# Kernel tuning notes

Measured on AMD Instinct MI355X. Metric: run time of the kernel, lower is better.

## Reference

```python
import jax, jax.numpy as jnp
import numpy as np

B, TQ, TK, D, F, H = 16, 256, 256, 256, 36, 8
DK = D // H          # dk = d // h
SF = int(np.sqrt(F)) # 6
MASK_VALUE = -1e30


def setup_inputs() -> dict:
    rng = jax.random.key(0)
    ks = jax.random.split(rng, 12)
    s = 0.05
    return {
        "query": jax.random.normal(ks[0], (B, TQ, D), jnp.float32),
        "key_ts": jax.random.normal(ks[1], (B, TK, D), jnp.float32),
        "value": jax.random.normal(ks[2], (B, TK, F), jnp.float32),
        "mask": (jax.random.uniform(ks[3], (B, TK, F)) < 0.5).astype(jnp.float32),
        "Wq": jax.random.normal(ks[4], (H, D, DK), jnp.float32) * s,
        "Wk": jax.random.normal(ks[5], (H, D, DK), jnp.float32) * s,
        "Wc": jax.random.normal(ks[6], (H, D), jnp.float32) * s,
        "bc": jnp.zeros((D,), jnp.float32),
        "Wo_1": jax.random.normal(ks[7], (F, SF), jnp.float32) * s,
        "bo_1": jnp.zeros((SF,), jnp.float32),
        "Wo_2": jax.random.normal(ks[8], (SF, 1), jnp.float32) * s,
        "bo_2": jnp.zeros((D,), jnp.float32),
    }


def reference(query, key_ts, value, mask, Wq, Wk, Wc, bc, Wo_1, bo_1, Wo_2, bo_2):
    # mask: [B, Tk, F] 0/1 missingness indicator -> broadcast as [B, 1, Tk, F]
    m = mask[:, None, :, :]
    heads = []
    for j in range(Wq.shape[0]):  # fixed small head loop (h=8)
        q = query @ Wq[j]                                  # [B, Tq, dk]
        k = key_ts @ Wk[j]                                 # [B, Tk, dk]
        A = jnp.einsum('bqd,bkd->bqk', q, k)[..., None]    # [B, Tq, Tk, 1] (no 1/sqrt(dk) scaling, as in original)
        A = m * A + (1.0 - m) * MASK_VALUE                 # [B, Tq, Tk, F]
        A = jax.nn.softmax(A, axis=-2)                     # softmax over Tk, per feature
        heads.append(jnp.einsum('bqkf,bkf->bqf', A, value))  # masked weighted sum
    latent = jnp.stack(heads, axis=-1)                     # [B, Tq, F, h]
    # permute (0,2,1,3) -> [B, F, Tq, h]; dot Wc[h,d] -> [B, F, Tq, d]
    latent = jnp.tanh(jnp.einsum('bqfh,hd->bfqd', latent, Wc) + bc)
    # permute (0,2,3,1) -> [B, Tq, d, F]; Wo_1: F -> sqrt(F)
    x = jnp.tanh(jnp.einsum('bfqd,fs->bqds', latent, Wo_1) + bo_1)
    # Wo_2: sqrt(F) -> 1, squeeze, add bo_2 -> [B, Tq, d]
    x = jnp.einsum('bqds,so->bqd', x, Wo_2) + bo_2
    return x
```

## Files before the change

### kernel.cpp

```cpp
#include <hip/hip_runtime.h>

#define NB 16
#define NTQ 256
#define NTK 256
#define ND 256
#define NF 36
#define NH 8
#define NDK 32
#define NSF 6

typedef __attribute__((ext_vector_type(8))) short short8;
typedef __attribute__((ext_vector_type(4))) float f32x4;
#define MFMA16(a,b,c) __builtin_amdgcn_mfma_f32_16x16x32_bf16(a,b,c,0,0,0)

#define WQTH_OFF 0u
#define WQTL_OFF (WQTH_OFF + 131072u)
#define WKTH_OFF (WQTH_OFF + 262144u)
#define WKTL_OFF (WQTH_OFF + 393216u)
#define RT_OFF   (WQTH_OFF + 524288u)
#define QPH_OFF  (2u*1024*1024)
#define QPL_OFF  (6u*1024*1024)
#define KPH_OFF  (10u*1024*1024)
#define KPL_OFF  (14u*1024*1024)
#define HD_OFF   (18u*1024*1024)

__device__ __forceinline__ short f2bf(float x){
    union { float f; unsigned u; } v; v.f = x;
    unsigned r = v.u + 0x7fffu + ((v.u >> 16) & 1u);
    return (short)(r >> 16);
}
__device__ __forceinline__ float bf2f(short s){
    union { float f; unsigned u; } v; v.u = ((unsigned)(unsigned short)s) << 16;
    return v.f;
}
__device__ __forceinline__ float fast_tanh(float x){
    float e = __expf(2.0f*x);
    return 1.0f - 2.0f/(e + 1.0f);
}
__device__ __forceinline__ short8 ld8(const short* p){ return *(const short8*)p; }

__device__ __forceinline__ void cvt8(const float* __restrict__ p, short8& h8, short8& l8){
    f32x4 a = *(const f32x4*)p;
    f32x4 c = *(const f32x4*)(p + 4);
    #pragma unroll
    for (int i = 0; i < 4; ++i){
        short h0 = f2bf(a[i]); h8[i]   = h0; l8[i]   = f2bf(a[i] - bf2f(h0));
        short h1 = f2bf(c[i]); h8[4+i] = h1; l8[4+i] = f2bf(c[i] - bf2f(h1));
    }
}

__global__ void imta_pack(const float* __restrict__ Wq, const float* __restrict__ Wk,
                          const float* __restrict__ mask, const float* __restrict__ value,
                          char* __restrict__ wsb){
    const int bid = blockIdx.x, tid = threadIdx.x;
    if (bid < 512){
        const int idx = bid*256 + tid;
        const int arr = idx >> 16, rem = idx & 65535;
        const int d = rem & 255, jdk = rem >> 8;
        const int jj = jdk >> 5, dk = jdk & 31;
        const float* __restrict__ W = arr ? Wk : Wq;
        float v = W[(jj*ND + d)*NDK + dk];
        short h = f2bf(v);
        short* oh = (short*)(wsb + (arr ? WKTH_OFF : WQTH_OFF));
        short* ol = (short*)(wsb + (arr ? WKTL_OFF : WQTL_OFF));
        oh[rem] = h; ol[rem] = f2bf(v - bf2f(h));
        return;
    }
    const int rb = bid - 512;
    const int x = rb & 15, b = rb >> 4;
    const int k = tid;
    short* rt = (short*)(wsb + RT_OFF) + b*80*256;
    #pragma unroll
    for (int r = 0; r < 5; ++r){
        const int fp = x*5 + r;
        const int f = fp >> 1;
        short o = 0;
        if (f < NF){
            float m = mask[(b*NTK + k)*NF + f];
            o = (fp & 1) ? f2bf(m) : f2bf(m * value[(b*NTK + k)*NF + f]);
        }
        rt[fp*256 + k] = o;
    }
}

__global__ __launch_bounds__(256, 8)
void imta_proj(const float* __restrict__ query, const float* __restrict__ key_ts,
               char* __restrict__ wsb){
    const int t0 = (blockIdx.x >> 2)*16, c0 = (blockIdx.x & 3)*64;
    const int side = blockIdx.y, b = blockIdx.z;
    const int tid = threadIdx.x, w = tid >> 6, lane = tid & 63;
    const int col = lane & 15, quad = lane >> 4;

    const float* __restrict__ X = side ? key_ts : query;
    const short* WH = (const short*)(wsb + (side ? WKTH_OFF : WQTH_OFF));
    const short* WL = (const short*)(wsb + (side ? WKTL_OFF : WQTL_OFF));
    short* OH = (short*)(wsb + (side ? KPH_OFF : QPH_OFF));
    short* OL = (short*)(wsb + (side ? KPL_OFF : QPL_OFF));

    const int n = c0 + w*16 + col;
    const float* xrow = X + (size_t)(b*NTQ + t0 + col)*ND;

    f32x4 acc = (f32x4)0.f;
    #pragma unroll
    for (int kb = 0; kb < 8; ++kb){
        const int dko = kb*32 + quad*8;
        short8 ah, al;
        cvt8(xrow + dko, ah, al);
        short8 bh = ld8(WH + n*ND + dko);
        short8 bl = ld8(WL + n*ND + dko);
        acc = MFMA16(al, bh, acc);
        acc = MFMA16(ah, bl, acc);
        acc = MFMA16(ah, bh, acc);
    }
    const int j = n >> 5, dk = n & 31;
    #pragma unroll
    for (int r = 0; r < 4; ++r){
        const int t = t0 + quad*4 + r;
        float v = acc[r];
        short h = f2bf(v);
        size_t o = (size_t)(((b*NH + j)*NTQ + t)*NDK + dk);
        OH[o] = h; OL[o] = f2bf(v - bf2f(h));
    }
}

__global__ __launch_bounds__(256, 8)
void imta_attn(char* __restrict__ wsb, const float* __restrict__ value){
    const int t0 = blockIdx.x*16;
    const int j = blockIdx.y, b = blockIdx.z;
    const int tid = threadIdx.x, w = tid >> 6, lane = tid & 63;
    const int col = lane & 15, quad = lane >> 4;
    __shared__ __align__(16) short sE[16*264];
    const short* QH = (const short*)(wsb + QPH_OFF) + (b*NH + j)*NTQ*NDK;
    const short* QL = (const short*)(wsb + QPL_OFF) + (b*NH + j)*NTQ*NDK;
    const short* KH = (const short*)(wsb + KPH_OFF) + (b*NH + j)*NTK*NDK;
    const short* KL = (const short*)(wsb + KPL_OFF) + (b*NH + j)*NTK*NDK;
    const short* RT = (const short*)(wsb + RT_OFF) + b*80*256;
    float* HD = (float*)(wsb + HD_OFF) + (b*NH + j)*NTQ*NF;

    short8 ah = ld8(QH + (t0 + col)*NDK + quad*8);
    short8 al = ld8(QL + (t0 + col)*NDK + quad*8);
    #pragma unroll
    for (int nt = 0; nt < 4; ++nt){
        const int key0 = w*64 + nt*16;
        short8 bh = ld8(KH + (key0 + col)*NDK + quad*8);
        short8 bl = ld8(KL + (key0 + col)*NDK + quad*8);
        f32x4 c = (f32x4)0.f;
        c = MFMA16(al, bh, c);
        c = MFMA16(ah, bl, c);
        c = MFMA16(ah, bh, c);
        const int key = key0 + col;
        #pragma unroll
        for (int r = 0; r < 4; ++r)
            sE[(quad*4 + r)*264 + key] = f2bf(__expf(c[r]));
    }
    __syncthreads();

    f32x4 accA = (f32x4)0.f, accB = (f32x4)0.f;
    #pragma unroll 2
    for (int kb = 0; kb < 8; ++kb){
        const int ko = kb*32 + quad*8;
        short8 a = *(const short8*)&sE[col*264 + ko];
        short8 bb = ld8(RT + (w*16 + col)*256 + ko);
        accA = MFMA16(a, bb, accA);
        if (w == 0){
            short8 b2 = ld8(RT + (64 + col)*256 + ko);
            accB = MFMA16(a, b2, accB);
        }
    }
    __syncthreads();
    float* sH = (float*)sE;
    #pragma unroll
    for (int r = 0; r < 4; ++r){
        float v = accA[r];
        float o = __shfl_xor(v, 1, 64);
        if (!(col & 1)){
            const int f = w*8 + (col >> 1);
            float num = v, den = o, h;
            if (den != 0.0f) h = num/den;
            else {
                float s = 0.f;
                for (int k = 0; k < NTK; ++k) s += value[(b*NTK + k)*NF + f];
                h = s * (1.0f/256.0f);
            }
            sH[(quad*4 + r)*40 + f] = h;
        }
    }
    if (w == 0){
        #pragma unroll
        for (int r = 0; r < 4; ++r){
            float v = accB[r];
            float o = __shfl_xor(v, 1, 64);
            if (!(col & 1)){
                const int f = 32 + (col >> 1);
                if (f < NF){
                    float num = v, den = o, h;
                    if (den != 0.0f) h = num/den;
                    else {
                        float s = 0.f;
                        for (int k = 0; k < NTK; ++k) s += value[(b*NTK + k)*NF + f];
                        h = s * (1.0f/256.0f);
                    }
                    sH[(quad*4 + r)*40 + f] = h;
                }
            }
        }
    }
    __syncthreads();
    for (int idx = tid; idx < 16*NF; idx += 256){
        const int q = idx/NF, f = idx - q*NF;
        HD[(t0 + q)*NF + f] = sH[q*40 + f];
    }
}

__global__ void imta_final(const float* __restrict__ Wc, const float* __restrict__ bc,
                           const float* __restrict__ Wo1, const float* __restrict__ bo1,
                           const float* __restrict__ Wo2, const float* __restrict__ bo2,
                           const float* __restrict__ hd, float* __restrict__ out){
    const int bq = blockIdx.x;
    const int b = bq >> 8, qq = bq & 255;
    const int tid = threadIdx.x;
    __shared__ float sh[NF*NH];
    __shared__ float sW1[NF*NSF];
    for (int t = tid; t < NF*NH; t += 256){
        int jj = t/NF, f = t - jj*NF;
        sh[t] = hd[((b*NH + jj)*NTQ + qq)*NF + f];
    }
    if (tid < NF*NSF) sW1[tid] = Wo1[tid];
    __syncthreads();
    const int d = tid;
    float wcr[8];
    #pragma unroll
    for (int h = 0; h < 8; ++h) wcr[h] = Wc[h*ND + d];
    const float bcd = bc[d];
    float a2[6];
    #pragma unroll
    for (int s = 0; s < 6; ++s) a2[s] = bo1[s];
    #pragma unroll
    for (int f4 = 0; f4 < NF; f4 += 4){
        float4 sv[8];
        #pragma unroll
        for (int h = 0; h < 8; ++h) sv[h] = *(const float4*)&sh[h*NF + f4];
        #pragma unroll
        for (int fi = 0; fi < 4; ++fi){
            float a = bcd;
            #pragma unroll
            for (int h = 0; h < 8; ++h)
                a = fmaf(reinterpret_cast<const float*>(&sv[h])[fi], wcr[h], a);
            float lf = fast_tanh(a);
            const int f = f4 + fi;
            #pragma unroll
            for (int s = 0; s < 6; ++s)
                a2[s] = fmaf(lf, sW1[f*NSF + s], a2[s]);
        }
    }
    float o = bo2[d];
    #pragma unroll
    for (int s = 0; s < 6; ++s)
        o = fmaf(fast_tanh(a2[s]), Wo2[s], o);
    out[(b*NTQ + qq)*ND + d] = o;
}

extern "C" void kernel_launch(void* const* d_in, const int* in_sizes, int n_in,
                              void* d_out, int out_size, void* d_ws, size_t ws_size,
                              hipStream_t stream){
    const float* query  = (const float*)d_in[0];
    const float* key_ts = (const float*)d_in[1];
    const float* value  = (const float*)d_in[2];
    const float* mask   = (const float*)d_in[3];
    const float* Wq     = (const float*)d_in[4];
    const float* Wk     = (const float*)d_in[5];
    const float* Wc     = (const float*)d_in[6];
    const float* bc     = (const float*)d_in[7];
    const float* Wo1    = (const float*)d_in[8];
    const float* bo1    = (const float*)d_in[9];
    const float* Wo2    = (const float*)d_in[10];
    const float* bo2    = (const float*)d_in[11];
    char* wsb  = (char*)d_ws;
    float* out = (float*)d_out;
    (void)in_sizes; (void)n_in; (void)out_size; (void)ws_size;

    imta_pack <<<dim3(768),      dim3(256), 0, stream>>>(Wq, Wk, mask, value, wsb);
    imta_proj <<<dim3(64, 2, 16),dim3(256), 0, stream>>>(query, key_ts, wsb);
    imta_attn <<<dim3(16, 8, 16),dim3(256), 0, stream>>>(wsb, value);
    imta_final<<<dim3(4096),     dim3(256), 0, stream>>>(Wc, bc, Wo1, bo1, Wo2, bo2,
                                                         (const float*)(wsb + HD_OFF), out);
}
```

Measured before the change: 163.5 us.

## Fuse four kernels into one persistent kernel with grid-wide barriers

Replaces the pack, projection, attention and final kernels with a single persistent kernel of 512 blocks that loops over the former work units. Phases are separated by atomic-counter grid barriers, and a memset clears the counters before each launch. This removes three kernel launch gaps and tail effects. In exchange, every phase runs on only 512 blocks, the barriers add spin-wait cost, and correctness relies on all 512 blocks being co-resident. The barrier also has a spin timeout that could let blocks proceed before the others arrive.

```diff
diff --git a/kernel.cpp b/kernel.cpp
--- a/kernel.cpp
+++ b/kernel.cpp
@@ -23,6 +23,9 @@
 #define KPH_OFF  (10u*1024*1024)
 #define KPL_OFF  (14u*1024*1024)
 #define HD_OFF   (18u*1024*1024)
+#define CNT_OFF  (24u*1024*1024)
+
+#define NBLK 512u
 
 __device__ __forceinline__ short f2bf(float x){
     union { float f; unsigned u; } v; v.f = x;
@@ -49,11 +52,35 @@
     }
 }
 
-__global__ void imta_pack(const float* __restrict__ Wq, const float* __restrict__ Wk,
-                          const float* __restrict__ mask, const float* __restrict__ value,
-                          char* __restrict__ wsb){
+__device__ __forceinline__ void gridbar(unsigned* cnt){
+    __syncthreads();
+    if (threadIdx.x == 0){
+        __threadfence();
+        __hip_atomic_fetch_add(cnt, 1u, __ATOMIC_ACQ_REL, __HIP_MEMORY_SCOPE_AGENT);
+        unsigned it = 0;
+        while (__hip_atomic_load(cnt, __ATOMIC_ACQUIRE, __HIP_MEMORY_SCOPE_AGENT) < NBLK
+               && ++it < (1u << 17))
+            __builtin_amdgcn_s_sleep(2);
+        __threadfence();
+    }
+    __syncthreads();
+}
+
+__global__ __launch_bounds__(256, 4)
+void imta_all(const float* __restrict__ query, const float* __restrict__ key_ts,
+              const float* __restrict__ value, const float* __restrict__ mask,
+              const float* __restrict__ Wq, const float* __restrict__ Wk,
+              const float* __restrict__ Wc, const float* __restrict__ bc,
+              const float* __restrict__ Wo1, const float* __restrict__ bo1,
+              const float* __restrict__ Wo2, const float* __restrict__ bo2,
+              char* __restrict__ wsb, float* __restrict__ out){
     const int bid = blockIdx.x, tid = threadIdx.x;
-    if (bid < 512){
+    const int w = tid >> 6, lane = tid & 63;
+    const int col = lane & 15, quad = lane >> 4;
+    unsigned* cnts = (unsigned*)(wsb + CNT_OFF);
+    __shared__ __align__(16) short sBuf[16*264];
+
+    {
         const int idx = bid*256 + tid;
         const int arr = idx >> 16, rem = idx & 65535;
         const int d = rem & 255, jdk = rem >> 8;
@@ -64,200 +91,203 @@
         short* oh = (short*)(wsb + (arr ? WKTH_OFF : WQTH_OFF));
         short* ol = (short*)(wsb + (arr ? WKTL_OFF : WQTL_OFF));
         oh[rem] = h; ol[rem] = f2bf(v - bf2f(h));
-        return;
-    }
-    const int rb = bid - 512;
-    const int x = rb & 15, b = rb >> 4;
-    const int k = tid;
-    short* rt = (short*)(wsb + RT_OFF) + b*80*256;
-    #pragma unroll
-    for (int r = 0; r < 5; ++r){
-        const int fp = x*5 + r;
-        const int f = fp >> 1;
-        short o = 0;
-        if (f < NF){
-            float m = mask[(b*NTK + k)*NF + f];
-            o = (fp & 1) ? f2bf(m) : f2bf(m * value[(b*NTK + k)*NF + f]);
-        }
-        rt[fp*256 + k] = o;
-    }
-}
-
-__global__ __launch_bounds__(256, 8)
-void imta_proj(const float* __restrict__ query, const float* __restrict__ key_ts,
-               char* __restrict__ wsb){
-    const int t0 = (blockIdx.x >> 2)*16, c0 = (blockIdx.x & 3)*64;
-    const int side = blockIdx.y, b = blockIdx.z;
-    const int tid = threadIdx.x, w = tid >> 6, lane = tid & 63;
-    const int col = lane & 15, quad = lane >> 4;
-
-    const float* __restrict__ X = side ? key_ts : query;
-    const short* WH = (const short*)(wsb + (side ? WKTH_OFF : WQTH_OFF));
-    const short* WL = (const short*)(wsb + (side ? WKTL_OFF : WQTL_OFF));
-    short* OH = (short*)(wsb + (side ? KPH_OFF : QPH_OFF));
-    short* OL = (short*)(wsb + (side ? KPL_OFF : QPL_OFF));
-
-    const int n = c0 + w*16 + col;
-    const float* xrow = X + (size_t)(b*NTQ + t0 + col)*ND;
-
-    f32x4 acc = (f32x4)0.f;
-    #pragma unroll
-    for (int kb = 0; kb < 8; ++kb){
-        const int dko = kb*32 + quad*8;
-        short8 ah, al;
-        cvt8(xrow + dko, ah, al);
-        short8 bh = ld8(WH + n*ND + dko);
-        short8 bl = ld8(WL + n*ND + dko);
-        acc = MFMA16(al, bh, acc);
-        acc = MFMA16(ah, bl, acc);
-        acc = MFMA16(ah, bh, acc);
-    }
-    const int j = n >> 5, dk = n & 31;
-    #pragma unroll
-    for (int r = 0; r < 4; ++r){
-        const int t = t0 + quad*4 + r;
-        float v = acc[r];
-        short h = f2bf(v);
-        size_t o = (size_t)(((b*NH + j)*NTQ + t)*NDK + dk);
-        OH[o] = h; OL[o] = f2bf(v - bf2f(h));
-    }
-}
-
-__global__ __launch_bounds__(256, 8)
-void imta_attn(char* __restrict__ wsb, const float* __restrict__ value){
-    const int t0 = blockIdx.x*16;
-    const int j = blockIdx.y, b = blockIdx.z;
-    const int tid = threadIdx.x, w = tid >> 6, lane = tid & 63;
-    const int col = lane & 15, quad = lane >> 4;
-    __shared__ __align__(16) short sE[16*264];
-    const short* QH = (const short*)(wsb + QPH_OFF) + (b*NH + j)*NTQ*NDK;
-    const short* QL = (const short*)(wsb + QPL_OFF) + (b*NH + j)*NTQ*NDK;
-    const short* KH = (const short*)(wsb + KPH_OFF) + (b*NH + j)*NTK*NDK;
-    const short* KL = (const short*)(wsb + KPL_OFF) + (b*NH + j)*NTK*NDK;
-    const short* RT = (const short*)(wsb + RT_OFF) + b*80*256;
-    float* HD = (float*)(wsb + HD_OFF) + (b*NH + j)*NTQ*NF;
-
-    short8 ah = ld8(QH + (t0 + col)*NDK + quad*8);
-    short8 al = ld8(QL + (t0 + col)*NDK + quad*8);
-    #pragma unroll
-    for (int nt = 0; nt < 4; ++nt){
-        const int key0 = w*64 + nt*16;
-        short8 bh = ld8(KH + (key0 + col)*NDK + quad*8);
-        short8 bl = ld8(KL + (key0 + col)*NDK + quad*8);
-        f32x4 c = (f32x4)0.f;
-        c = MFMA16(al, bh, c);
-        c = MFMA16(ah, bl, c);
-        c = MFMA16(ah, bh, c);
-        const int key = key0 + col;
-        #pragma unroll
-        for (int r = 0; r < 4; ++r)
-            sE[(quad*4 + r)*264 + key] = f2bf(__expf(c[r]));
-    }
-    __syncthreads();
-
-    f32x4 accA = (f32x4)0.f, accB = (f32x4)0.f;
-    #pragma unroll 2
-    for (int kb = 0; kb < 8; ++kb){
-        const int ko = kb*32 + quad*8;
-        short8 a = *(const short8*)&sE[col*264 + ko];
-        short8 bb = ld8(RT + (w*16 + col)*256 + ko);
-        accA = MFMA16(a, bb, accA);
-        if (w == 0){
-            short8 b2 = ld8(RT + (64 + col)*256 + ko);
-            accB = MFMA16(a, b2, accB);
-        }
-    }
-    __syncthreads();
-    float* sH = (float*)sE;
-    #pragma unroll
-    for (int r = 0; r < 4; ++r){
-        float v = accA[r];
-        float o = __shfl_xor(v, 1, 64);
-        if (!(col & 1)){
-            const int f = w*8 + (col >> 1);
-            float num = v, den = o, h;
-            if (den != 0.0f) h = num/den;
-            else {
-                float s = 0.f;
-                for (int k = 0; k < NTK; ++k) s += value[(b*NTK + k)*NF + f];
-                h = s * (1.0f/256.0f);
-            }
-            sH[(quad*4 + r)*40 + f] = h;
-        }
-    }
-    if (w == 0){
+    }
+    if (bid < 256){
+        const int x = bid & 15, b = bid >> 4;
+        const int k = tid;
+        short* rt = (short*)(wsb + RT_OFF) + b*80*256;
+        #pragma unroll
+        for (int r = 0; r < 5; ++r){
+            const int fp = x*5 + r;
+            const int f = fp >> 1;
+            short o = 0;
+            if (f < NF){
+                float m = mask[(b*NTK + k)*NF + f];
+                o = (fp & 1) ? f2bf(m) : f2bf(m * value[(b*NTK + k)*NF + f]);
+            }
+            rt[fp*256 + k] = o;
+        }
+    }
+    gridbar(cnts + 0);
+
+    for (int i = 0; i < 4; ++i){
+        const unsigned u = (unsigned)bid + NBLK*i;
+        const int x = u & 63, side = (u >> 6) & 1, b = u >> 7;
+        const int t0 = (x >> 2)*16, c0 = (x & 3)*64;
+        const float* __restrict__ X = side ? key_ts : query;
+        const short* WH = (const short*)(wsb + (side ? WKTH_OFF : WQTH_OFF));
+        const short* WL = (const short*)(wsb + (side ? WKTL_OFF : WQTL_OFF));
+        short* OH = (short*)(wsb + (side ? KPH_OFF : QPH_OFF));
+        short* OL = (short*)(wsb + (side ? KPL_OFF : QPL_OFF));
+
+        const int n = c0 + w*16 + col;
+        const float* xrow = X + (size_t)(b*NTQ + t0 + col)*ND;
+
+        f32x4 acc = (f32x4)0.f;
+        #pragma unroll
+        for (int kb = 0; kb < 8; ++kb){
+            const int dko = kb*32 + quad*8;
+            short8 ah, al;
+            cvt8(xrow + dko, ah, al);
+            short8 bh = ld8(WH + n*ND + dko);
+            short8 bl = ld8(WL + n*ND + dko);
+            acc = MFMA16(al, bh, acc);
+            acc = MFMA16(ah, bl, acc);
+            acc = MFMA16(ah, bh, acc);
+        }
+        const int j = n >> 5, dk = n & 31;
         #pragma unroll
         for (int r = 0; r < 4; ++r){
-            float v = accB[r];
+            const int t = t0 + quad*4 + r;
+            float v = acc[r];
+            short h = f2bf(v);
+            size_t o = (size_t)(((b*NH + j)*NTQ + t)*NDK + dk);
+            OH[o] = h; OL[o] = f2bf(v - bf2f(h));
+        }
+    }
+    gridbar(cnts + 1);
+
+    for (int i = 0; i < 4; ++i){
+        const unsigned u = (unsigned)bid + NBLK*i;
+        const int xq = u & 15, j = (u >> 4) & 7, b = u >> 7;
+        const int t0 = xq*16;
+        short* const sE = sBuf;
+        const short* QH = (const short*)(wsb + QPH_OFF) + (b*NH + j)*NTQ*NDK;
+        const short* QL = (const short*)(wsb + QPL_OFF) + (b*NH + j)*NTQ*NDK;
+        const short* KH = (const short*)(wsb + KPH_OFF) + (b*NH + j)*NTK*NDK;
+        const short* KL = (const short*)(wsb + KPL_OFF) + (b*NH + j)*NTK*NDK;
+        const short* RT = (const short*)(wsb + RT_OFF) + b*80*256;
+        float* HD = (float*)(wsb + HD_OFF) + (b*NH + j)*NTQ*NF;
+
+        __syncthreads();
+        short8 ah = ld8(QH + (t0 + col)*NDK + quad*8);
+        short8 al = ld8(QL + (t0 + col)*NDK + quad*8);
+        #pragma unroll
+        for (int nt = 0; nt < 4; ++nt){
+            const int key0 = w*64 + nt*16;
+            short8 bh = ld8(KH + (key0 + col)*NDK + quad*8);
+            short8 bl = ld8(KL + (key0 + col)*NDK + quad*8);
+            f32x4 c = (f32x4)0.f;
+            c = MFMA16(al, bh, c);
+            c = MFMA16(ah, bl, c);
+            c = MFMA16(ah, bh, c);
+            const int key = key0 + col;
+            #pragma unroll
+            for (int r = 0; r < 4; ++r)
+                sE[(quad*4 + r)*264 + key] = f2bf(__expf(c[r]));
+        }
+        __syncthreads();
+
+        f32x4 accA = (f32x4)0.f, accB = (f32x4)0.f;
+        #pragma unroll 2
+        for (int kb = 0; kb < 8; ++kb){
+            const int ko = kb*32 + quad*8;
+            short8 a = *(const short8*)&sE[col*264 + ko];
+            short8 bb = ld8(RT + (w*16 + col)*256 + ko);
+            accA = MFMA16(a, bb, accA);
+            if (w == 0){
+                short8 b2 = ld8(RT + (64 + col)*256 + ko);
+                accB = MFMA16(a, b2, accB);
+            }
+        }
+        __syncthreads();
+        float* sH = (float*)sBuf;
+        #pragma unroll
+        for (int r = 0; r < 4; ++r){
+            float v = accA[r];
             float o = __shfl_xor(v, 1, 64);
             if (!(col & 1)){
-                const int f = 32 + (col >> 1);
-                if (f < NF){
-                    float num = v, den = o, h;
-                    if (den != 0.0f) h = num/den;
-                    else {
-                        float s = 0.f;
-                        for (int k = 0; k < NTK; ++k) s += value[(b*NTK + k)*NF + f];
-                        h = s * (1.0f/256.0f);
+                const int f = w*8 + (col >> 1);
+                float num = v, den = o, h;
+                if (den != 0.0f) h = num/den;
+                else {
+                    float s = 0.f;
+                    for (int k = 0; k < NTK; ++k) s += value[(b*NTK + k)*NF + f];
+                    h = s * (1.0f/256.0f);
+                }
+                sH[(quad*4 + r)*40 + f] = h;
+            }
+        }
+        if (w == 0){
+            #pragma unroll
+            for (int r = 0; r < 4; ++r){
+                float v = accB[r];
+                float o = __shfl_xor(v, 1, 64);
+                if (!(col & 1)){
+                    const int f = 32 + (col >> 1);
+                    if (f < NF){
+                        float num = v, den = o, h;
+                        if (den != 0.0f) h = num/den;
+                        else {
+                            float s = 0.f;
+                            for (int k = 0; k < NTK; ++k) s += value[(b*NTK + k)*NF + f];
+                            h = s * (1.0f/256.0f);
+                        }
+                        sH[(quad*4 + r)*40 + f] = h;
                     }
-                    sH[(quad*4 + r)*40 + f] = h;
                 }
             }
         }
-    }
-    __syncthreads();
-    for (int idx = tid; idx < 16*NF; idx += 256){
-        const int q = idx/NF, f = idx - q*NF;
-        HD[(t0 + q)*NF + f] = sH[q*40 + f];
-    }
-}
-
-__global__ void imta_final(const float* __restrict__ Wc, const float* __restrict__ bc,
-                           const float* __restrict__ Wo1, const float* __restrict__ bo1,
-                           const float* __restrict__ Wo2, const float* __restrict__ bo2,
-                           const float* __restrict__ hd, float* __restrict__ out){
-    const int bq = blockIdx.x;
-    const int b = bq >> 8, qq = bq & 255;
-    const int tid = threadIdx.x;
-    __shared__ float sh[NF*NH];
-    __shared__ float sW1[NF*NSF];
-    for (int t = tid; t < NF*NH; t += 256){
-        int jj = t/NF, f = t - jj*NF;
-        sh[t] = hd[((b*NH + jj)*NTQ + qq)*NF + f];
-    }
-    if (tid < NF*NSF) sW1[tid] = Wo1[tid];
-    __syncthreads();
-    const int d = tid;
-    float wcr[8];
-    #pragma unroll
-    for (int h = 0; h < 8; ++h) wcr[h] = Wc[h*ND + d];
-    const float bcd = bc[d];
-    float a2[6];
-    #pragma unroll
-    for (int s = 0; s < 6; ++s) a2[s] = bo1[s];
-    #pragma unroll
-    for (int f4 = 0; f4 < NF; f4 += 4){
-        float4 sv[8];
-        #pragma unroll
-        for (int h = 0; h < 8; ++h) sv[h] = *(const float4*)&sh[h*NF + f4];
-        #pragma unroll
-        for (int fi = 0; fi < 4; ++fi){
-            float a = bcd;
-            #pragma unroll
-            for (int h = 0; h < 8; ++h)
-                a = fmaf(reinterpret_cast<const float*>(&sv[h])[fi], wcr[h], a);
-            float lf = fast_tanh(a);
-            const int f = f4 + fi;
+        __syncthreads();
+        for (int idx = tid; idx < 16*NF; idx += 256){
+            const int q = idx/NF, f = idx - q*NF;
+            HD[(t0 + q)*NF + f] = sH[q*40 + f];
+        }
+    }
+    gridbar(cnts + 2);
+
+    {
+        const float* hd = (const float*)(wsb + HD_OFF);
+        const int d = tid;
+        float* shf = (float*)sBuf;
+        float* sW1 = shf + NF*NH;
+        if (tid < NF*NSF) sW1[tid] = Wo1[tid];
+        float wcr[8];
+        #pragma unroll
+        for (int h = 0; h < 8; ++h) wcr[h] = Wc[h*ND + d];
+        const float bcd = bc[d];
+        float bo1r[6], wo2r[6];
+        #pragma unroll
+        for (int s = 0; s < 6; ++s){ bo1r[s] = bo1[s]; wo2r[s] = Wo2[s]; }
+        const float bo2d = bo2[d];
+
+        for (int i = 0; i < 8; ++i){
+            const int unit = bid*8 + i;
+            const int b = unit >> 8, qq = unit & 255;
+            __syncthreads();
+            for (int t = tid; t < NF*NH; t += 256){
+                int jj = t/NF, f = t - jj*NF;
+                shf[t] = hd[((b*NH + jj)*NTQ + qq)*NF + f];
+            }
+            __syncthreads();
+            float a2[6];
+            #pragma unroll
+            for (int s = 0; s < 6; ++s) a2[s] = bo1r[s];
+            #pragma unroll
+            for (int f4 = 0; f4 < NF; f4 += 4){
+                float4 sv[8];
+                #pragma unroll
+                for (int h = 0; h < 8; ++h) sv[h] = *(const float4*)&shf[h*NF + f4];
+                #pragma unroll
+                for (int fi = 0; fi < 4; ++fi){
+                    float a = bcd;
+                    #pragma unroll
+                    for (int h = 0; h < 8; ++h)
+                        a = fmaf(reinterpret_cast<const float*>(&sv[h])[fi], wcr[h], a);
+                    float lf = fast_tanh(a);
+                    const int f = f4 + fi;
+                    #pragma unroll
+                    for (int s = 0; s < 6; ++s)
+                        a2[s] = fmaf(lf, sW1[f*NSF + s], a2[s]);
+                }
+            }
+            float o = bo2d;
             #pragma unroll
             for (int s = 0; s < 6; ++s)
-                a2[s] = fmaf(lf, sW1[f*NSF + s], a2[s]);
-        }
-    }
-    float o = bo2[d];
-    #pragma unroll
-    for (int s = 0; s < 6; ++s)
-        o = fmaf(fast_tanh(a2[s]), Wo2[s], o);
-    out[(b*NTQ + qq)*ND + d] = o;
+                o = fmaf(fast_tanh(a2[s]), wo2r[s], o);
+            out[(b*NTQ + qq)*ND + d] = o;
+        }
+    }
 }
 
 extern "C" void kernel_launch(void* const* d_in, const int* in_sizes, int n_in,
@@ -279,9 +309,8 @@
     float* out = (float*)d_out;
     (void)in_sizes; (void)n_in; (void)out_size; (void)ws_size;
 
-    imta_pack <<<dim3(768),      dim3(256), 0, stream>>>(Wq, Wk, mask, value, wsb);
-    imta_proj <<<dim3(64, 2, 16),dim3(256), 0, stream>>>(query, key_ts, wsb);
-    imta_attn <<<dim3(16, 8, 16),dim3(256), 0, stream>>>(wsb, value);
-    imta_final<<<dim3(4096),     dim3(256), 0, stream>>>(Wc, bc, Wo1, bo1, Wo2, bo2,
-                                                         (const float*)(wsb + HD_OFF), out);
-}
+    hipMemsetAsync(wsb + CNT_OFF, 0, 256, stream);
+    imta_all<<<dim3(NBLK), dim3(256), 0, stream>>>(query, key_ts, value, mask,
+                                                   Wq, Wk, Wc, bc, Wo1, bo1, Wo2, bo2,
+                                                   wsb, out);
+}
```

After: 374.1 us. 129% more time.

## Fuse weight packing into projection kernel, staging split-bf16 weights in LDS

Applied to the files above, without the earlier changes.

Removes the separate pack kernel. Each projection block now converts its own head's Wq/Wk slice to hi/lo bf16 in shared memory, and the mask/value packing runs as extra blocks of the same launch. Each block computes a 64x32 tile per head with two accumulators instead of reading pre-transposed global weights. This saves one kernel launch and a global round trip of the packed weights. In exchange, every block redundantly converts 8K weights and occupancy is lowered to 4 blocks.

```diff
diff --git a/kernel.cpp b/kernel.cpp
--- a/kernel.cpp
+++ b/kernel.cpp
@@ -13,11 +13,7 @@
 typedef __attribute__((ext_vector_type(4))) float f32x4;
 #define MFMA16(a,b,c) __builtin_amdgcn_mfma_f32_16x16x32_bf16(a,b,c,0,0,0)
 
-#define WQTH_OFF 0u
-#define WQTL_OFF (WQTH_OFF + 131072u)
-#define WKTH_OFF (WQTH_OFF + 262144u)
-#define WKTL_OFF (WQTH_OFF + 393216u)
-#define RT_OFF   (WQTH_OFF + 524288u)
+#define RT_OFF   524288u
 #define QPH_OFF  (2u*1024*1024)
 #define QPL_OFF  (6u*1024*1024)
 #define KPH_OFF  (10u*1024*1024)
@@ -49,77 +45,88 @@
     }
 }
 
-__global__ void imta_pack(const float* __restrict__ Wq, const float* __restrict__ Wk,
-                          const float* __restrict__ mask, const float* __restrict__ value,
-                          char* __restrict__ wsb){
+__global__ __launch_bounds__(256, 4)
+void imta_proj(const float* __restrict__ query, const float* __restrict__ key_ts,
+               const float* __restrict__ Wq, const float* __restrict__ Wk,
+               const float* __restrict__ mask, const float* __restrict__ value,
+               char* __restrict__ wsb){
     const int bid = blockIdx.x, tid = threadIdx.x;
-    if (bid < 512){
-        const int idx = bid*256 + tid;
-        const int arr = idx >> 16, rem = idx & 65535;
-        const int d = rem & 255, jdk = rem >> 8;
-        const int jj = jdk >> 5, dk = jdk & 31;
-        const float* __restrict__ W = arr ? Wk : Wq;
-        float v = W[(jj*ND + d)*NDK + dk];
-        short h = f2bf(v);
-        short* oh = (short*)(wsb + (arr ? WKTH_OFF : WQTH_OFF));
-        short* ol = (short*)(wsb + (arr ? WKTL_OFF : WQTL_OFF));
-        oh[rem] = h; ol[rem] = f2bf(v - bf2f(h));
+    if (bid >= 1024){
+        const int rb = bid - 1024;
+        const int x = rb & 15, b = rb >> 4;
+        const int k = tid;
+        short* rt = (short*)(wsb + RT_OFF) + b*80*256;
+        #pragma unroll
+        for (int r = 0; r < 5; ++r){
+            const int fp = x*5 + r;
+            const int f = fp >> 1;
+            short o = 0;
+            if (f < NF){
+                float m = mask[(b*NTK + k)*NF + f];
+                o = (fp & 1) ? f2bf(m) : f2bf(m * value[(b*NTK + k)*NF + f]);
+            }
+            rt[fp*256 + k] = o;
+        }
         return;
     }
-    const int rb = bid - 512;
-    const int x = rb & 15, b = rb >> 4;
-    const int k = tid;
-    short* rt = (short*)(wsb + RT_OFF) + b*80*256;
-    #pragma unroll
-    for (int r = 0; r < 5; ++r){
-        const int fp = x*5 + r;
-        const int f = fp >> 1;
-        short o = 0;
-        if (f < NF){
-            float m = mask[(b*NTK + k)*NF + f];
-            o = (fp & 1) ? f2bf(m) : f2bf(m * value[(b*NTK + k)*NF + f]);
-        }
-        rt[fp*256 + k] = o;
-    }
-}
-
-__global__ __launch_bounds__(256, 8)
-void imta_proj(const float* __restrict__ query, const float* __restrict__ key_ts,
-               char* __restrict__ wsb){
-    const int t0 = (blockIdx.x >> 2)*16, c0 = (blockIdx.x & 3)*64;
-    const int side = blockIdx.y, b = blockIdx.z;
-    const int tid = threadIdx.x, w = tid >> 6, lane = tid & 63;
+    const int b = bid >> 6, side = (bid >> 5) & 1, j = (bid >> 2) & 7;
+    const int t0 = (bid & 3)*64;
+    const int w = tid >> 6, lane = tid & 63;
     const int col = lane & 15, quad = lane >> 4;
 
+    __shared__ __align__(16) short sW[2*32*264];
+    short* const sWH = sW;
+    short* const sWL = sW + 32*264;
+
     const float* __restrict__ X = side ? key_ts : query;
-    const short* WH = (const short*)(wsb + (side ? WKTH_OFF : WQTH_OFF));
-    const short* WL = (const short*)(wsb + (side ? WKTL_OFF : WQTL_OFF));
+    const float* __restrict__ W = (side ? Wk : Wq) + (size_t)j*ND*NDK;
     short* OH = (short*)(wsb + (side ? KPH_OFF : QPH_OFF));
     short* OL = (short*)(wsb + (side ? KPL_OFF : QPL_OFF));
 
-    const int n = c0 + w*16 + col;
-    const float* xrow = X + (size_t)(b*NTQ + t0 + col)*ND;
-
-    f32x4 acc = (f32x4)0.f;
+    {
+        const int dk0 = (tid & 7)*4, dbase = tid >> 3;
+        #pragma unroll
+        for (int it = 0; it < 8; ++it){
+            const int d = dbase + it*32;
+            f32x4 wv = *(const f32x4*)(W + (size_t)d*NDK + dk0);
+            #pragma unroll
+            for (int i = 0; i < 4; ++i){
+                short h = f2bf(wv[i]);
+                sWH[(dk0 + i)*264 + d] = h;
+                sWL[(dk0 + i)*264 + d] = f2bf(wv[i] - bf2f(h));
+            }
+        }
+    }
+    __syncthreads();
+
+    const int row = t0 + w*16 + col;
+    const float* xrow = X + (size_t)(b*NTQ + row)*ND;
+    f32x4 acc[2]; acc[0] = (f32x4)0.f; acc[1] = (f32x4)0.f;
     #pragma unroll
     for (int kb = 0; kb < 8; ++kb){
         const int dko = kb*32 + quad*8;
         short8 ah, al;
         cvt8(xrow + dko, ah, al);
-        short8 bh = ld8(WH + n*ND + dko);
-        short8 bl = ld8(WL + n*ND + dko);
-        acc = MFMA16(al, bh, acc);
-        acc = MFMA16(ah, bl, acc);
-        acc = MFMA16(ah, bh, acc);
-    }
-    const int j = n >> 5, dk = n & 31;
-    #pragma unroll
-    for (int r = 0; r < 4; ++r){
-        const int t = t0 + quad*4 + r;
-        float v = acc[r];
-        short h = f2bf(v);
-        size_t o = (size_t)(((b*NH + j)*NTQ + t)*NDK + dk);
-        OH[o] = h; OL[o] = f2bf(v - bf2f(h));
+        #pragma unroll
+        for (int nt = 0; nt < 2; ++nt){
+            short8 bh = *(const short8*)&sWH[(nt*16 + col)*264 + dko];
+            short8 bl = *(const short8*)&sWL[(nt*16 + col)*264 + dko];
+            acc[nt] = MFMA16(al, bh, acc[nt]);
+            acc[nt] = MFMA16(ah, bl, acc[nt]);
+            acc[nt] = MFMA16(ah, bh, acc[nt]);
+        }
+    }
+    #pragma unroll
+    for (int nt = 0; nt < 2; ++nt){
+        const int dk = nt*16 + col;
+        #pragma unroll
+        for (int r = 0; r < 4; ++r){
+            const int t = t0 + w*16 + quad*4 + r;
+            float v = acc[nt][r];
+            short h = f2bf(v);
+            size_t o = (size_t)(((b*NH + j)*NTQ + t)*NDK + dk);
+            OH[o] = h; OL[o] = f2bf(v - bf2f(h));
+        }
     }
 }
 
@@ -279,8 +286,7 @@
     float* out = (float*)d_out;
     (void)in_sizes; (void)n_in; (void)out_size; (void)ws_size;
 
-    imta_pack <<<dim3(768),      dim3(256), 0, stream>>>(Wq, Wk, mask, value, wsb);
-    imta_proj <<<dim3(64, 2, 16),dim3(256), 0, stream>>>(query, key_ts, wsb);
+    imta_proj <<<dim3(1280),     dim3(256), 0, stream>>>(query, key_ts, Wq, Wk, mask, value, wsb);
     imta_attn <<<dim3(16, 8, 16),dim3(256), 0, stream>>>(wsb, value);
     imta_final<<<dim3(4096),     dim3(256), 0, stream>>>(Wc, bc, Wo1, bo1, Wo2, bo2,
                                                          (const float*)(wsb + HD_OFF), out);
```

New measurement: 141.9 us, median of 2. 13.2% less time.
